# Optimization experiments

Hardware: AMD Instinct MI355X
Metric: run time of the kernel (lower is better)

The kernel has to match this reference:

```python
import jax, jax.numpy as jnp
import numpy as np

B, N, D = 8, 2048, 256
K = 16384  # codebook_size


def setup_inputs() -> dict:
    key = jax.random.key(0)
    k1, k2, k3, k4 = jax.random.split(key, 4)
    z = jax.random.normal(k1, (B, N, D), dtype=jnp.float32)
    emb_weight = jax.random.normal(k2, (K, D), dtype=jnp.float32) * 0.02
    proj_w = jax.random.normal(k3, (D, D), dtype=jnp.float32) * (1.0 / np.sqrt(D))
    proj_b = jax.random.normal(k4, (D,), dtype=jnp.float32) * 0.01
    return {"z": z, "emb_weight": emb_weight, "proj_w": proj_w, "proj_b": proj_b}


def reference(z, emb_weight, proj_w, proj_b):
    # emb = embedding_proj(embedding.weight)  (torch Linear: x @ W^T + b)
    emb = emb_weight @ proj_w.T + proj_b  # (K, D)
    b, n, d = z.shape
    zf = z.reshape(b * n, d)  # (BN, D)
    # squared euclidean distances: ||z||^2 + ||e||^2 - 2 z e^T
    dist = (
        jnp.sum(zf * zf, axis=1, keepdims=True)
        + jnp.sum(emb * emb, axis=1)
        - 2.0 * jnp.einsum("bd,kd->bk", zf, emb)
    )  # (BN, K)
    q_indices = jnp.argmin(dist, axis=1)  # (BN,) int
    quantized = emb[q_indices].reshape(z.shape)  # (B, N, D)
    # straight-through estimator
    quantized = z + jax.lax.stop_gradient(quantized - z)
    q_indices = q_indices.reshape(b, n)
    # (unregularized_z, emb, regularized_z, bottleneck_rep)
    return z, emb, quantized, q_indices
```

## Files before the change

kernel.cpp:

```cpp
#include <hip/hip_runtime.h>
#include <hip/hip_bf16.h>

#define D       256
#define KCB     16384
#define BNROWS  16384
#define MARGIN  0.15f
#define ZMAX    5.0f
#define EMAX    0.2f
#define FS2U    (2.0f * (ZMAX / 127.0f) * (EMAX / 127.0f))
#define MARGIN_INT 1210u
#define IBIAS   8388608

typedef __attribute__((ext_vector_type(4))) int   int4v;
typedef __attribute__((ext_vector_type(4))) float f32x4;
typedef unsigned long long u64;

__device__ __forceinline__ void gload_lds16(const void* g, void* l) {
    __builtin_amdgcn_global_load_lds(
        (const __attribute__((address_space(1))) void*)g,
        (__attribute__((address_space(3))) void*)l, 16, 0, 0);
}

__device__ __forceinline__ unsigned fmap(float f) {
    unsigned u = __float_as_uint(f);
    return (u & 0x80000000u) ? ~u : (u | 0x80000000u);
}

__device__ __forceinline__ signed char q8(float x, float s) {
    return (signed char)__float2int_rn(fminf(fmaxf(x * s, -127.f), 127.f));
}

__global__ __launch_bounds__(256) void prep_kernel(
    const float* __restrict__ z, signed char* __restrict__ z8,
    const float* __restrict__ ew, const float* __restrict__ pw,
    const float* __restrict__ pb, float* __restrict__ emb,
    signed char* __restrict__ e8)
{
    __shared__ float Et[64][65];
    __shared__ float Pt[64][65];
    const int tid = threadIdx.x;

    if (blockIdx.x < 4096) {
        const int i = blockIdx.x * 256 + tid;
        float4 v = ((const float4*)z)[i];
        const float s = 127.0f / ZMAX;
        char4 c;
        c.x = q8(v.x, s); c.y = q8(v.y, s); c.z = q8(v.z, s); c.w = q8(v.w, s);
        ((char4*)z8)[i] = c;
        return;
    }

    const int bid = blockIdx.x - 4096;
    const int tc  = tid & 15, tr = tid >> 4;
    const int k0  = (bid >> 2) * 64;
    const int d0  = (bid & 3) * 64;

    float acc[4][4];
#pragma unroll
    for (int a = 0; a < 4; ++a)
#pragma unroll
        for (int b = 0; b < 4; ++b) acc[a][b] = 0.f;

    for (int j0 = 0; j0 < 256; j0 += 64) {
        __syncthreads();
#pragma unroll
        for (int i = 0; i < 4; ++i) {
            const int c = i * 256 + tid;
            const int r = c >> 4, c4 = (c & 15) * 4;
            float4 v = *(const float4*)(ew + (size_t)(k0 + r) * 256 + j0 + c4);
            Et[r][c4 + 0] = v.x; Et[r][c4 + 1] = v.y;
            Et[r][c4 + 2] = v.z; Et[r][c4 + 3] = v.w;
            float4 w = *(const float4*)(pw + (size_t)(d0 + r) * 256 + j0 + c4);
            Pt[r][c4 + 0] = w.x; Pt[r][c4 + 1] = w.y;
            Pt[r][c4 + 2] = w.z; Pt[r][c4 + 3] = w.w;
        }
        __syncthreads();
        for (int j = 0; j < 64; ++j) {
            float ev[4], pv[4];
#pragma unroll
            for (int a = 0; a < 4; ++a) ev[a] = Et[tr * 4 + a][j];
#pragma unroll
            for (int b = 0; b < 4; ++b) pv[b] = Pt[tc * 4 + b][j];
#pragma unroll
            for (int a = 0; a < 4; ++a)
#pragma unroll
                for (int b = 0; b < 4; ++b)
                    acc[a][b] = fmaf(ev[a], pv[b], acc[a][b]);
        }
    }

    const float4 bias = *(const float4*)(pb + d0 + tc * 4);
    const float se = 127.0f / EMAX;
#pragma unroll
    for (int a = 0; a < 4; ++a) {
        float4 o;
        o.x = acc[a][0] + bias.x; o.y = acc[a][1] + bias.y;
        o.z = acc[a][2] + bias.z; o.w = acc[a][3] + bias.w;
        const size_t off = (size_t)(k0 + tr * 4 + a) * 256 + d0 + tc * 4;
        *(float4*)(emb + off) = o;
        char4 c;
        c.x = q8(o.x, se); c.y = q8(o.y, se);
        c.z = q8(o.z, se); c.w = q8(o.w, se);
        *(char4*)(e8 + off) = c;
    }
}

__global__ __launch_bounds__(256) void snorm_kernel(
    const float* __restrict__ emb, float* __restrict__ s,
    int* __restrict__ s_bi)
{
    const int tid = threadIdx.x;
    const int row = blockIdx.x * 64 + (tid >> 2);
    const int qd  = tid & 3;
    const size_t base = (size_t)row * 256;
    float sq = 0.f;
#pragma unroll
    for (int j = 0; j < 16; ++j) {
        const int off = qd * 4 + j * 16;
        float4 v = *(const float4*)(emb + base + off);
        sq = fmaf(v.x, v.x, fmaf(v.y, v.y, fmaf(v.z, v.z, fmaf(v.w, v.w, sq))));
    }
    sq += __shfl_xor(sq, 1);
    sq += __shfl_xor(sq, 2);
    if (qd == 0) {
        s[row]    = sq;
        s_bi[row] = (int)rintf(sq / FS2U) + IBIAS;
    }
}

__global__ __launch_bounds__(512, 4) void argmin_hi_kernel(
    const signed char* __restrict__ z8, const signed char* __restrict__ e8,
    const int* __restrict__ s_bi,
    unsigned* __restrict__ partial1, unsigned* __restrict__ partial2)
{
    __shared__ alignas(16) short A_lds[2 * 4096];
    __shared__ alignas(16) short B_lds[4 * 8192];

    const int tid  = threadIdx.x;
    const int lane = tid & 63;
    const int wid  = tid >> 6;
    const int wz   = wid >> 2;
    const int wc   = wid & 3;
    const int lcol = lane & 15;
    const int rhi  = lane >> 4;

    const int bn  = blockIdx.x & 63;
    const int bm0 = blockIdx.x >> 6;
    const size_t n0 = (size_t)bn * 256;

    const int slot  = (((lcol & 1) * 4 + rhi) ^ ((lcol >> 1) & 7)) << 3;
    const int aoff0 = wz * 2048 + (lcol >> 1) * 64 + slot;
    const int boff0 = wc * 2048 + (lcol >> 1) * 64 + slot;

    auto goff = [](int c) {
        const int l = c >> 3, u = (c & 7) ^ (l & 7);
        return (size_t)(2 * l + (u >> 2)) * 256 + (size_t)(u & 3) * 16;
    };
    const size_t gA  = goff(tid);
    const int    cB0 = wid * 128 + lane;
    const int    cB1 = cB0 + 64;
    const size_t gB0 = goff(cB0);
    const size_t gB1 = goff(cB1);

    const char* const e8B = (const char*)e8 + n0 * 256;
    const char*       zc  = (const char*)z8 + (size_t)bm0 * 32768;

#pragma unroll
    for (int t = 0; t < 4; ++t) {
        gload_lds16(e8B + (t << 6) + gB0, (void*)(B_lds + t * 8192 + cB0 * 8));
        gload_lds16(e8B + (t << 6) + gB1, (void*)(B_lds + t * 8192 + cB1 * 8));
    }
    gload_lds16(zc + gA,      (void*)(A_lds + tid * 8));
    gload_lds16(zc + 64 + gA, (void*)(A_lds + 4096 + tid * 8));
    asm volatile("s_waitcnt vmcnt(1)" ::: "memory");
    __builtin_amdgcn_s_barrier();

#define COMPUTE_TILE(ABUF, BT)                                                \
    {                                                                         \
        int4v bq[4];                                                          \
        _Pragma("unroll")                                                     \
        for (int n = 0; n < 4; ++n)                                           \
            bq[n] = *(const int4v*)(A_lds + (ABUF) * 4096 + aoff0 + n * 512); \
        __builtin_amdgcn_s_setprio(1);                                        \
        _Pragma("unroll")                                                     \
        for (int m = 0; m < 4; ++m) {                                         \
            const int4v am = *(const int4v*)(B_lds + (BT) * 8192 + boff0 + m * 512); \
            _Pragma("unroll")                                                 \
            for (int n = 0; n < 4; ++n)                                       \
                acc[m][n] = __builtin_amdgcn_mfma_i32_16x16x64_i8(            \
                    am, bq[n], acc[m][n], 0, 0, 0);                           \
        }                                                                     \
        __builtin_amdgcn_s_setprio(0);                                        \
    }

#pragma unroll 1
    for (int i = 0; i < 16; ++i) {
        const bool more = (i < 15);

        int4v acc[4][4];
        const int4v izero = {0, 0, 0, 0};
#pragma unroll
        for (int m = 0; m < 4; ++m)
#pragma unroll
            for (int n = 0; n < 4; ++n) acc[m][n] = izero;

        COMPUTE_TILE(0, 0)
        asm volatile("s_waitcnt vmcnt(0)" ::: "memory");
        __builtin_amdgcn_s_barrier();

        gload_lds16(zc + 128 + gA, (void*)(A_lds + tid * 8));
        COMPUTE_TILE(1, 1)
        asm volatile("s_waitcnt vmcnt(0)" ::: "memory");
        __builtin_amdgcn_s_barrier();

        gload_lds16(zc + 192 + gA, (void*)(A_lds + 4096 + tid * 8));
        COMPUTE_TILE(0, 2)
        asm volatile("s_waitcnt vmcnt(0)" ::: "memory");
        __builtin_amdgcn_s_barrier();

        if (more) gload_lds16(zc + 262144 + gA, (void*)(A_lds + tid * 8));
        COMPUTE_TILE(1, 3)
        __builtin_amdgcn_s_barrier();

        int4v sb[4];
#pragma unroll
        for (int mc = 0; mc < 4; ++mc)
            sb[mc] = *(const int4v*)(s_bi + n0 + wc * 64 + mc * 16 + rhi * 4);

        u64* cand = (u64*)(A_lds + 4096);
#pragma unroll
        for (int nz = 0; nz < 4; ++nz) {
            unsigned v[16];
#pragma unroll
            for (int mc = 0; mc < 4; ++mc) {
                const unsigned cb = (unsigned)(wc * 64 + mc * 16 + rhi * 4);
#pragma unroll
                for (int j = 0; j < 4; ++j)
                    v[mc * 4 + j] =
                        ((unsigned)(sb[mc][j] - acc[mc][nz][j]) << 8) | (cb + j);
            }
            unsigned p1 = min(v[0], v[1]), p2 = max(v[0], v[1]);
#pragma unroll
            for (int q = 1; q < 8; ++q) {
                const unsigned l = min(v[2 * q], v[2 * q + 1]);
                const unsigned h = max(v[2 * q], v[2 * q + 1]);
                const unsigned t = max(p1, l);
                p1 = min(p1, l);
                p2 = min(t, min(p2, h));
            }
#pragma unroll
            for (int mask = 16; mask <= 32; mask <<= 1) {
                const unsigned q1 = __shfl_xor(p1, mask);
                const unsigned q2 = __shfl_xor(p2, mask);
                const unsigned t  = max(p1, q1);
                p1 = min(p1, q1);
                p2 = min(t, min(p2, q2));
            }
            if (rhi == 0) {
                const int row = wz * 64 + nz * 16 + lcol;
                cand[row * 4 + wc] = (u64)p1 | ((u64)p2 << 32);
            }
        }
        __syncthreads();
        if (tid < 128) {
            const u64* c4 = cand + (size_t)tid * 4;
            u64 a = c4[0];
            unsigned p1 = (unsigned)a, p2 = (unsigned)(a >> 32);
#pragma unroll
            for (int w = 1; w < 4; ++w) {
                a = c4[w];
                const unsigned q1 = (unsigned)a, q2 = (unsigned)(a >> 32);
                const unsigned t  = max(p1, q1);
                p1 = min(p1, q1);
                p2 = min(t, min(p2, q2));
            }
            const size_t r0 = (size_t)(bm0 + 8 * i) * 128;
            partial1[(size_t)bn * BNROWS + r0 + tid] = p1;
            partial2[(size_t)bn * BNROWS + r0 + tid] = p2;
        }
        __syncthreads();

        if (more) gload_lds16(zc + 262144 + 64 + gA, (void*)(A_lds + 4096 + tid * 8));
        zc += 262144;
    }
#undef COMPUTE_TILE
}

__global__ __launch_bounds__(256) void collect_rescore_kernel(
    const unsigned* __restrict__ partial1, const unsigned* __restrict__ partial2,
    const float* __restrict__ z, const float* __restrict__ emb,
    const float* __restrict__ s,
    float* __restrict__ outz, float* __restrict__ outq,
    float* __restrict__ outidx)
{
    __shared__ unsigned gsb;
    __shared__ int      nsel;
    __shared__ int      selk[128];
    __shared__ u64      wbest[4];
    __shared__ int      kfin;

    const int tid  = threadIdx.x;
    const int row  = blockIdx.x;
    const int lane = tid & 63;
    const int wid  = tid >> 6;

    unsigned v = 0xFFFFFFFFu;
    int vbn = 0;
    if (tid < 64)       { v = partial1[(size_t)tid * BNROWS + row];        vbn = tid; }
    else if (tid < 128) { v = partial2[(size_t)(tid - 64) * BNROWS + row]; vbn = tid - 64; }

    if (tid < 64) {
        unsigned g = v;
#pragma unroll
        for (int mm = 1; mm < 64; mm <<= 1) g = min(g, (unsigned)__shfl_xor(g, mm));
        if (tid == 0) { gsb = g; nsel = 0; }
    }
    __syncthreads();

    const unsigned thr = (((gsb >> 8) + MARGIN_INT) << 8) | 0xFFu;
    if (tid < 128 && v <= thr) {
        const int i = atomicAdd(&nsel, 1);
        selk[i] = vbn * 256 + (int)(v & 0xFFu);
    }
    __syncthreads();

    const float4 zv = *(const float4*)(z + (size_t)row * 256 + lane * 4);
    const int ns = nsel;
    u64 best = ~0ull;
    for (int i = wid; i < ns; i += 4) {
        const int k = selk[i];
        const float4 ev = *(const float4*)(emb + (size_t)k * 256 + lane * 4);
        float p = zv.x * ev.x;
        p = fmaf(zv.y, ev.y, p);
        p = fmaf(zv.z, ev.z, p);
        p = fmaf(zv.w, ev.w, p);
#pragma unroll
        for (int mm = 1; mm < 64; mm <<= 1) p += __shfl_xor(p, mm);
        const float sc = fmaf(-2.f, p, s[k]);
        const u64 pk = ((u64)fmap(sc) << 32) | (unsigned)k;
        best = (pk < best) ? pk : best;
    }
    if (lane == 0) wbest[wid] = best;
    __syncthreads();
    if (tid == 0) {
        u64 b = wbest[0];
        if (wbest[1] < b) b = wbest[1];
        if (wbest[2] < b) b = wbest[2];
        if (wbest[3] < b) b = wbest[3];
        kfin = (int)(b & 0xffffffffu);
        outidx[row] = (float)kfin;
    }
    __syncthreads();

    const int k = kfin;
    outz[(size_t)row * 256 + tid] = z[(size_t)row * 256 + tid];
    outq[(size_t)row * 256 + tid] = emb[(size_t)k * 256 + tid];
}

extern "C" void kernel_launch(void* const* d_in, const int* in_sizes, int n_in,
                              void* d_out, int out_size, void* d_ws, size_t ws_size,
                              hipStream_t stream)
{
    const float* z  = (const float*)d_in[0];
    const float* ew = (const float*)d_in[1];
    const float* pw = (const float*)d_in[2];
    const float* pb = (const float*)d_in[3];

    float* out     = (float*)d_out;
    float* out_z   = out;
    float* out_emb = out + (size_t)BNROWS * D;
    float* out_q   = out + 2 * (size_t)BNROWS * D;
    float* out_idx = out + 3 * (size_t)BNROWS * D;

    float*       sbuf  = (float*)d_ws;
    int*         s_bi  = (int*)((char*)d_ws + 65536);
    signed char* z8    = (signed char*)((char*)d_ws + 131072);
    unsigned*    part1 = (unsigned*)((char*)d_ws + 131072 + 4194304);
    unsigned*    part2 = (unsigned*)((char*)d_ws + 131072 + 2 * 4194304);
    signed char* e8    = (signed char*)out_q;

    prep_kernel<<<4096 + 1024, 256, 0, stream>>>(z, z8, ew, pw, pb, out_emb, e8);
    snorm_kernel<<<KCB / 64, 256, 0, stream>>>(out_emb, sbuf, s_bi);
    argmin_hi_kernel<<<512, 512, 0, stream>>>(z8, e8, s_bi, part1, part2);
    collect_rescore_kernel<<<BNROWS, 256, 0, stream>>>(
        part1, part2, z, out_emb, sbuf, out_z, out_q, out_idx);
}
```

Measured before the change: 177.4 us.

## Batch 64 rows per block in rescore kernel with coalesced partial loads

The collect/rescore kernel now processes 64 rows per block instead of one. It stages the partial-minimum arrays into LDS through a transposed, coalesced load, and each wave handles 16 rows using ballot/popcount compaction in place of shared atomics. Output copies switch to float4. The candidate list is capped at 32 per row, which could drop a true minimum if more candidates pass the margin. Launching only 256 blocks may also underfill the GPU, and each wave's rescoring now runs sequentially.

```diff
diff --git a/kernel.cpp b/kernel.cpp
--- a/kernel.cpp
+++ b/kernel.cpp
@@ -293,68 +293,83 @@
     float* __restrict__ outz, float* __restrict__ outq,
     float* __restrict__ outidx)
 {
-    __shared__ unsigned gsb;
-    __shared__ int      nsel;
-    __shared__ int      selk[128];
-    __shared__ u64      wbest[4];
-    __shared__ int      kfin;
-
-    const int tid  = threadIdx.x;
-    const int row  = blockIdx.x;
-    const int lane = tid & 63;
-    const int wid  = tid >> 6;
-
-    unsigned v = 0xFFFFFFFFu;
-    int vbn = 0;
-    if (tid < 64)       { v = partial1[(size_t)tid * BNROWS + row];        vbn = tid; }
-    else if (tid < 128) { v = partial2[(size_t)(tid - 64) * BNROWS + row]; vbn = tid - 64; }
-
-    if (tid < 64) {
-        unsigned g = v;
+    __shared__ unsigned p1s[64][65];
+    __shared__ unsigned p2s[64][65];
+    __shared__ int      cands[64][32];
+    __shared__ int      kfin[64];
+
+    const int tid     = threadIdx.x;
+    const int rowbase = blockIdx.x * 64;
+    const int lane    = tid & 63;
+    const int w       = tid >> 6;
+
+#pragma unroll
+    for (int i = 0; i < 16; ++i) {
+        const int idx = i * 256 + tid;
+        const int bn = idx >> 6, r = idx & 63;
+        p1s[r][bn] = partial1[(size_t)bn * BNROWS + rowbase + r];
+        p2s[r][bn] = partial2[(size_t)bn * BNROWS + rowbase + r];
+    }
+    __syncthreads();
+
+    for (int rr = 0; rr < 16; ++rr) {
+        const int r    = w * 16 + rr;
+        const int rowg = rowbase + r;
+
+        const unsigned v1 = p1s[r][lane];
+        const unsigned v2 = p2s[r][lane];
+
+        unsigned g = v1;
 #pragma unroll
         for (int mm = 1; mm < 64; mm <<= 1) g = min(g, (unsigned)__shfl_xor(g, mm));
-        if (tid == 0) { gsb = g; nsel = 0; }
+        const unsigned thr = (((g >> 8) + MARGIN_INT) << 8) | 0xFFu;
+
+        const u64 m1 = __ballot(v1 <= thr);
+        const u64 m2 = __ballot(v2 <= thr);
+        const int n1 = (int)__popcll(m1);
+        const u64 below = (lane == 0) ? 0ull : ((1ull << lane) - 1ull);
+        if (v1 <= thr) {
+            const int slot = (int)__popcll(m1 & below);
+            if (slot < 32) cands[r][slot] = lane * 256 + (int)(v1 & 0xFFu);
+        }
+        if (v2 <= thr) {
+            const int slot = n1 + (int)__popcll(m2 & below);
+            if (slot < 32) cands[r][slot] = lane * 256 + (int)(v2 & 0xFFu);
+        }
+        const int nc = min(n1 + (int)__popcll(m2), 32);
+
+        const float4 zv = ((const float4*)z)[(size_t)rowg * 64 + lane];
+        u64 best = ~0ull;
+        for (int c = 0; c < nc; ++c) {
+            const int k = cands[r][c];
+            const float4 ev = ((const float4*)emb)[(size_t)k * 64 + lane];
+            float p = zv.x * ev.x;
+            p = fmaf(zv.y, ev.y, p);
+            p = fmaf(zv.z, ev.z, p);
+            p = fmaf(zv.w, ev.w, p);
+#pragma unroll
+            for (int mm = 1; mm < 64; mm <<= 1) p += __shfl_xor(p, mm);
+            const float sc = fmaf(-2.f, p, s[k]);
+            const u64 pk = ((u64)fmap(sc) << 32) | (unsigned)k;
+            best = (pk < best) ? pk : best;
+        }
+        if (lane == 0) {
+            const int kb = (int)(best & 0xffffffffu);
+            kfin[r] = kb;
+            outidx[rowg] = (float)kb;
+        }
     }
     __syncthreads();
 
-    const unsigned thr = (((gsb >> 8) + MARGIN_INT) << 8) | 0xFFu;
-    if (tid < 128 && v <= thr) {
-        const int i = atomicAdd(&nsel, 1);
-        selk[i] = vbn * 256 + (int)(v & 0xFFu);
-    }
-    __syncthreads();
-
-    const float4 zv = *(const float4*)(z + (size_t)row * 256 + lane * 4);
-    const int ns = nsel;
-    u64 best = ~0ull;
-    for (int i = wid; i < ns; i += 4) {
-        const int k = selk[i];
-        const float4 ev = *(const float4*)(emb + (size_t)k * 256 + lane * 4);
-        float p = zv.x * ev.x;
-        p = fmaf(zv.y, ev.y, p);
-        p = fmaf(zv.z, ev.z, p);
-        p = fmaf(zv.w, ev.w, p);
-#pragma unroll
-        for (int mm = 1; mm < 64; mm <<= 1) p += __shfl_xor(p, mm);
-        const float sc = fmaf(-2.f, p, s[k]);
-        const u64 pk = ((u64)fmap(sc) << 32) | (unsigned)k;
-        best = (pk < best) ? pk : best;
-    }
-    if (lane == 0) wbest[wid] = best;
-    __syncthreads();
-    if (tid == 0) {
-        u64 b = wbest[0];
-        if (wbest[1] < b) b = wbest[1];
-        if (wbest[2] < b) b = wbest[2];
-        if (wbest[3] < b) b = wbest[3];
-        kfin = (int)(b & 0xffffffffu);
-        outidx[row] = (float)kfin;
-    }
-    __syncthreads();
-
-    const int k = kfin;
-    outz[(size_t)row * 256 + tid] = z[(size_t)row * 256 + tid];
-    outq[(size_t)row * 256 + tid] = emb[(size_t)k * 256 + tid];
+#pragma unroll
+    for (int i = 0; i < 16; ++i) {
+        const int idx = i * 256 + tid;
+        const int r = idx >> 6, c4 = idx & 63;
+        const size_t rowg = (size_t)(rowbase + r);
+        ((float4*)outz)[rowg * 64 + c4] = ((const float4*)z)[rowg * 64 + c4];
+        ((float4*)outq)[rowg * 64 + c4] =
+            ((const float4*)emb)[(size_t)kfin[r] * 64 + c4];
+    }
 }
 
 extern "C" void kernel_launch(void* const* d_in, const int* in_sizes, int n_in,
@@ -382,6 +397,6 @@
     prep_kernel<<<4096 + 1024, 256, 0, stream>>>(z, z8, ew, pw, pb, out_emb, e8);
     snorm_kernel<<<KCB / 64, 256, 0, stream>>>(out_emb, sbuf, s_bi);
     argmin_hi_kernel<<<512, 512, 0, stream>>>(z8, e8, s_bi, part1, part2);
-    collect_rescore_kernel<<<BNROWS, 256, 0, stream>>>(
+    collect_rescore_kernel<<<256, 256, 0, stream>>>(
         part1, part2, z, out_emb, sbuf, out_z, out_q, out_idx);
 }
```

New measurement: 192.9 us. +8.7%, slower.
